# Kernel optimization log

Measured on AMD Instinct MI355X. Metric: run time of the kernel, lower is better.

The kernel has to match this reference:

```python
import jax, jax.numpy as jnp
import numpy as np
import math

B, Q_LEN, K_LEN = 8, 512, 512
D_MODEL, H = 512, 8
DK = D_MODEL // H


def setup_inputs() -> dict:
    key = jax.random.key(0)
    ks = jax.random.split(key, 12)
    inp = {
        "query": jax.random.normal(ks[0], (B, Q_LEN, D_MODEL), jnp.float32),
        "key": jax.random.normal(ks[1], (B, K_LEN, D_MODEL), jnp.float32),
        "value": jax.random.normal(ks[2], (B, K_LEN, D_MODEL), jnp.float32),
        "relative_embeddings": jax.random.normal(ks[3], (K_LEN, Q_LEN, D_MODEL), jnp.float32),
        # causal mask: 1 = attend, 0 = masked
        "mask": jnp.tril(jnp.ones((Q_LEN, K_LEN), dtype=bool)),
        "Wq": jax.random.normal(ks[4], (D_MODEL, D_MODEL), jnp.float32) / math.sqrt(D_MODEL),
        "Wk": jax.random.normal(ks[5], (D_MODEL, D_MODEL), jnp.float32) / math.sqrt(D_MODEL),
        "Wv": jax.random.normal(ks[6], (D_MODEL, D_MODEL), jnp.float32) / math.sqrt(D_MODEL),
        "Wo": jax.random.normal(ks[7], (D_MODEL, D_MODEL), jnp.float32) / math.sqrt(D_MODEL),
        "Wr": jax.random.normal(ks[8], (D_MODEL, D_MODEL), jnp.float32) / math.sqrt(D_MODEL),
        "u": jax.random.normal(ks[9], (H, DK), jnp.float32),
        "v": jax.random.normal(ks[10], (H, DK), jnp.float32),
    }
    return inp


def reference(query, key, value, relative_embeddings, mask, Wq, Wk, Wv, Wo, Wr, u, v):
    b, q_len, d_model = query.shape
    k_len = key.shape[1]
    # torch nn.Linear(x) = x @ W.T (bias=False)
    Qh = (query @ Wq.T).reshape(b, q_len, H, DK).transpose(0, 2, 1, 3)   # bhqd
    Kh = (key @ Wk.T).reshape(b, k_len, H, DK).transpose(0, 2, 1, 3)     # bhkd
    Vh = (value @ Wv.T).reshape(b, k_len, H, DK).transpose(0, 2, 1, 3)   # bhkd
    # relative position projection: (k_len, q_len, d_model)
    R = relative_embeddings @ Wr.T
    # view(k,q,H,dk).permute(2,1,0,3) -> (H, q, k, dk)
    Rh = R.reshape(k_len, q_len, H, DK).transpose(2, 1, 0, 3)
    # content score: (Q + u) K^T
    content = jnp.einsum("bhqd,bhkd->bhqk", Qh + u[None, :, None, :], Kh)
    # position score: (Q + v) R^T, R per-head per-query
    position = jnp.einsum("bhqd,hqkd->bhqk", Qh + v[None, :, None, :], Rh)
    scores = (content + position) / math.sqrt(DK)
    scores = jnp.where(mask[None, None, :, :], scores, -1e9)
    weights = jax.nn.softmax(scores, axis=-1)  # dropout is identity in eval
    out = jnp.einsum("bhqk,bhkd->bhqd", weights, Vh)
    out = out.transpose(0, 2, 1, 3).reshape(b, q_len, d_model)
    out = out @ Wo.T
    return (out, weights)
```

## Files before the change

### kernel.cpp

```cpp
#include <hip/hip_runtime.h>

#define BATCH   8
#define SEQ     512
#define DMODEL  512
#define NHEAD   8
#define DKH     64

typedef __attribute__((ext_vector_type(8))) short bf16x8;
typedef __attribute__((ext_vector_type(4))) float f32x4;

__device__ __forceinline__ short f2bf(float f) {
    union { float f; unsigned u; } v; v.f = f;
    unsigned r = v.u + 0x7FFFu + ((v.u >> 16) & 1u);
    return (short)(r >> 16);
}
__device__ __forceinline__ float bf2f(short s) {
    union { unsigned u; float f; } v; v.u = ((unsigned)(unsigned short)s) << 16;
    return v.f;
}

#define LDK 40

__device__ __forceinline__ void stage_f32(const float* __restrict__ base,
                                          int rstride, short* lds, int tid) {
    int r = tid >> 2, c = (tid & 3) << 3;
    const float* p = base + (size_t)r * rstride + c;
    float4 x = *(const float4*)p;
    float4 y = *(const float4*)(p + 4);
    union { short s[8]; bf16x8 v; } o;
    o.s[0] = f2bf(x.x); o.s[1] = f2bf(x.y); o.s[2] = f2bf(x.z); o.s[3] = f2bf(x.w);
    o.s[4] = f2bf(y.x); o.s[5] = f2bf(y.y); o.s[6] = f2bf(y.z); o.s[7] = f2bf(y.w);
    *(bf16x8*)(lds + r * LDK + c) = o.v;
}

__device__ __forceinline__ void stage_bf16(const short* __restrict__ base,
                                           int rstride, short* lds, int tid) {
    int r = tid >> 2, c = (tid & 3) << 3;
    bf16x8 v = *(const bf16x8*)(base + (size_t)r * rstride + c);
    *(bf16x8*)(lds + r * LDK + c) = v;
}

__device__ __forceinline__ void mma_tile(const short* As, const short* Bs,
                                         int lane, int wm, int wn, f32x4 acc[2][2]) {
    int lo = lane & 15, hi = lane >> 4;
    bf16x8 a0 = *(const bf16x8*)(As + (wm * 32 + lo) * LDK + hi * 8);
    bf16x8 a1 = *(const bf16x8*)(As + (wm * 32 + 16 + lo) * LDK + hi * 8);
    bf16x8 b0 = *(const bf16x8*)(Bs + (wn * 32 + lo) * LDK + hi * 8);
    bf16x8 b1 = *(const bf16x8*)(Bs + (wn * 32 + 16 + lo) * LDK + hi * 8);
    acc[0][0] = __builtin_amdgcn_mfma_f32_16x16x32_bf16(a0, b0, acc[0][0], 0, 0, 0);
    acc[0][1] = __builtin_amdgcn_mfma_f32_16x16x32_bf16(a0, b1, acc[0][1], 0, 0, 0);
    acc[1][0] = __builtin_amdgcn_mfma_f32_16x16x32_bf16(a1, b0, acc[1][0], 0, 0, 0);
    acc[1][1] = __builtin_amdgcn_mfma_f32_16x16x32_bf16(a1, b1, acc[1][1], 0, 0, 0);
}

__global__ __launch_bounds__(256) void qkvw_kernel(
        const float* __restrict__ query, const float* __restrict__ key_,
        const float* __restrict__ value,
        const float* __restrict__ Wq, const float* __restrict__ Wk,
        const float* __restrict__ Wv, const float* __restrict__ Wr,
        const float* __restrict__ uvec, const float* __restrict__ vvec,
        short* __restrict__ Qu, short* __restrict__ Qv,
        short* __restrict__ Kh, short* __restrict__ Vt,
        short* __restrict__ Wrt) {
    __shared__ short As[64 * LDK], Bs[64 * LDK];
    int f = blockIdx.x, tid = threadIdx.x;
    if (f >= 1536) {
        int base = (f - 1536) * 1024;
        #pragma unroll
        for (int j = 0; j < 4; j++) {
            int idx = base + j * 256 + tid;
            int n = idx >> 9, m = idx & 511;
            Wrt[idx] = f2bf(Wr[(size_t)m * 512 + n]);
        }
        return;
    }
    int i = f >> 3;
    int nt = i & 7;
    int gm = (f & 7) * 24 + (i >> 3);
    int mode = gm >> 6, mt = gm & 63;
    const float* x = mode == 0 ? query : (mode == 1 ? key_ : value);
    const float* W = mode == 0 ? Wq : (mode == 1 ? Wk : Wv);
    int lane = tid & 63, w = tid >> 6, wm = w >> 1, wn = w & 1;
    const float* Abase = x + (size_t)mt * 64 * DMODEL;
    const float* Bbase = W + (size_t)nt * 64 * DMODEL;
    f32x4 acc[2][2] = {};
    for (int kt = 0; kt < DMODEL; kt += 32) {
        __syncthreads();
        stage_f32(Abase + kt, DMODEL, As, tid);
        stage_f32(Bbase + kt, DMODEL, Bs, tid);
        __syncthreads();
        mma_tile(As, Bs, lane, wm, wn, acc);
    }
    int lo = lane & 15, hi = lane >> 4;
    for (int fm = 0; fm < 2; fm++)
        for (int fn = 0; fn < 2; fn++)
            for (int r = 0; r < 4; r++) {
                int m = mt * 64 + wm * 32 + fm * 16 + hi * 4 + r;
                int n = nt * 64 + wn * 32 + fn * 16 + lo;
                float val = acc[fm][fn][r];
                int b = m >> 9, s = m & 511, h = n >> 6, d = n & 63;
                if (mode == 0) {
                    size_t idx = ((size_t)(b * NHEAD + h) * SEQ + s) * DKH + d;
                    Qu[idx] = f2bf(val + uvec[n]);
                    Qv[idx] = f2bf(val + vvec[n]);
                } else if (mode == 1) {
                    Kh[((size_t)(b * NHEAD + h) * SEQ + s) * DKH + d] = f2bf(val);
                } else {
                    Vt[((size_t)(b * NHEAD + h) * DKH + d) * SEQ + s] = f2bf(val);
                }
            }
}

__global__ __launch_bounds__(256) void tc_kernel(const short* __restrict__ Qv,
                                                 const short* __restrict__ Wrt,
                                                 short* __restrict__ T2,
                                                 const short* __restrict__ Qu,
                                                 const short* __restrict__ Kh,
                                                 float* __restrict__ scores) {
    __shared__ short As[64 * LDK], Bs[64 * LDK];
    int f0 = blockIdx.x, tid = threadIdx.x;
    int lane = tid & 63, w = tid >> 6, wm = w >> 1, wn = w & 1;
    int lo = lane & 15, hi = lane >> 4;
    if (f0 < 4096) {
        int f = f0;
        int i = f >> 3;
        int nt = i & 7;
        int mh = (f & 7) * 64 + (i >> 3);
        int mt = mh >> 3, h = mh & 7;
        int m0 = mt * 64, b = m0 >> 9, q0 = m0 & 511;
        const short* Abase = Qv + ((size_t)(b * NHEAD + h) * SEQ + q0) * DKH;
        const short* Bbase = Wrt + (size_t)nt * 64 * DMODEL + h * DKH;
        f32x4 acc[2][2] = {};
        for (int kt = 0; kt < DKH; kt += 32) {
            __syncthreads();
            stage_bf16(Abase + kt, DKH, As, tid);
            stage_bf16(Bbase + kt, DMODEL, Bs, tid);
            __syncthreads();
            mma_tile(As, Bs, lane, wm, wn, acc);
        }
        int bh = b * NHEAD + h;
        for (int fm = 0; fm < 2; fm++)
            for (int fn = 0; fn < 2; fn++)
                for (int r = 0; r < 4; r++) {
                    int q = q0 + wm * 32 + fm * 16 + hi * 4 + r;
                    int n = nt * 64 + wn * 32 + fn * 16 + lo;
                    T2[((size_t)q * 64 + bh) * DMODEL + n] = f2bf(acc[fm][fn][r]);
                }
    } else {
        int i = f0 - 4096;
        int x = i & 7, j = i >> 3;
        int bhl = j / 36, t = j % 36;
        int bh = x * 8 + bhl;
        int qt = 0, base = 0;
        #pragma unroll
        for (int s = 1; s <= 7; s++) { if (t >= base + qt + 1) { base += qt + 1; qt++; } }
        int kt_ = t - base;
        const short* Abase = Qu + ((size_t)bh * SEQ + qt * 64) * DKH;
        const short* Bbase = Kh + ((size_t)bh * SEQ + kt_ * 64) * DKH;
        f32x4 acc[2][2] = {};
        for (int kt = 0; kt < DKH; kt += 32) {
            __syncthreads();
            stage_bf16(Abase + kt, DKH, As, tid);
            stage_bf16(Bbase + kt, DKH, Bs, tid);
            __syncthreads();
            mma_tile(As, Bs, lane, wm, wn, acc);
        }
        for (int fm = 0; fm < 2; fm++)
            for (int fn = 0; fn < 2; fn++)
                for (int r = 0; r < 4; r++) {
                    int q = qt * 64 + wm * 32 + fm * 16 + hi * 4 + r;
                    int k = kt_ * 64 + wn * 32 + fn * 16 + lo;
                    scores[((size_t)bh * SEQ + q) * SEQ + k] = acc[fm][fn][r];
                }
    }
}

__global__ __launch_bounds__(1024) void position_kernel(const short* __restrict__ T2,
                                                        const float* __restrict__ rel,
                                                        float* __restrict__ scores) {
    int bk = blockIdx.x;
    int x = bk & 7, idx = bk >> 3;
    int q = (idx < 32) ? (idx * 8 + x) : (511 - ((idx - 32) * 8 + x));
    __shared__ short Tl[64 * 512];
    int tid = threadIdx.x, w = tid >> 6, lane = tid & 63;
    const short* Tq = T2 + (size_t)q * (64 * DMODEL);
    #pragma unroll
    for (int it = 0; it < 4; ++it) {
        int chunk = it * 1024 + tid;
        int r = chunk >> 6, c = chunk & 63;
        bf16x8 v = *(const bf16x8*)(Tq + (size_t)chunk * 8);
        *(bf16x8*)(Tl + r * 512 + (c ^ (r & 7)) * 8) = v;
    }
    __syncthreads();
    int kbase = w * 32;
    if (kbase > q) return;
    int lo = lane & 15, hi = lane >> 4;
    const float* relq = rel + ((size_t)kbase * SEQ + q) * DMODEL;
    f32x4 acc[4][2] = {};
    for (int n = 0; n < DMODEL; n += 32) {
        bf16x8 a[4];
        #pragma unroll
        for (int fm = 0; fm < 4; fm++) {
            int rr = fm * 16 + lo;
            int g = ((n >> 3) + hi) ^ (rr & 7);
            a[fm] = *(const bf16x8*)(Tl + rr * 512 + g * 8);
        }
        bf16x8 bfrag[2];
        #pragma unroll
        for (int fk = 0; fk < 2; fk++) {
            const float* p = relq + (size_t)(fk * 16 + lo) * (SEQ * DMODEL) + n + hi * 8;
            float4 xv = *(const float4*)p;
            float4 yv = *(const float4*)(p + 4);
            union { short s[8]; bf16x8 v; } o;
            o.s[0] = f2bf(xv.x); o.s[1] = f2bf(xv.y); o.s[2] = f2bf(xv.z); o.s[3] = f2bf(xv.w);
            o.s[4] = f2bf(yv.x); o.s[5] = f2bf(yv.y); o.s[6] = f2bf(yv.z); o.s[7] = f2bf(yv.w);
            bfrag[fk] = o.v;
        }
        #pragma unroll
        for (int fm = 0; fm < 4; fm++) {
            acc[fm][0] = __builtin_amdgcn_mfma_f32_16x16x32_bf16(a[fm], bfrag[0], acc[fm][0], 0, 0, 0);
            acc[fm][1] = __builtin_amdgcn_mfma_f32_16x16x32_bf16(a[fm], bfrag[1], acc[fm][1], 0, 0, 0);
        }
    }
    #pragma unroll
    for (int fm = 0; fm < 4; fm++)
        #pragma unroll
        for (int fk = 0; fk < 2; fk++)
            #pragma unroll
            for (int r = 0; r < 4; r++) {
                int bh = fm * 16 + hi * 4 + r;
                int k = kbase + fk * 16 + lo;
                scores[((size_t)bh * SEQ + q) * SEQ + k] += acc[fm][fk][r];
            }
}

#define PSTR 520
__global__ __launch_bounds__(256) void pv_sm_kernel(float* __restrict__ scores,
                                                    const short* __restrict__ Vt,
                                                    short* __restrict__ attn) {
    __shared__ short Ps[64 * PSTR];
    __shared__ float invS_lds[64];
    int f = blockIdx.x;
    int i = f >> 3;
    int bhl, qt;
    if (i < 32) { bhl = i >> 3;            qt = i & 7; }
    else        { bhl = 4 + ((i - 32) >> 3); qt = 7 - (i & 7); }
    int bh = (f & 7) * 8 + bhl;
    int tid = threadIdx.x, lane = tid & 63, w = tid >> 6, wm = w >> 1, wn = w & 1;
    int kmax = (qt + 1) * 64;
    int r = tid >> 2, c4 = tid & 3;
    int q = qt * 64 + r;
    int cc = c4 * 8;
    float* row = scores + ((size_t)bh * SEQ + q) * SEQ;
    float S = 0.f;
    for (int kt = 0; kt < kmax; kt += 32) {
        float4 x = *(const float4*)(row + kt + cc);
        float4 y = *(const float4*)(row + kt + cc + 4);
        float p0 = (kt + cc + 0 <= q) ? __expf(x.x * 0.125f) : 0.f;
        float p1 = (kt + cc + 1 <= q) ? __expf(x.y * 0.125f) : 0.f;
        float p2 = (kt + cc + 2 <= q) ? __expf(x.z * 0.125f) : 0.f;
        float p3 = (kt + cc + 3 <= q) ? __expf(x.w * 0.125f) : 0.f;
        float p4 = (kt + cc + 4 <= q) ? __expf(y.x * 0.125f) : 0.f;
        float p5 = (kt + cc + 5 <= q) ? __expf(y.y * 0.125f) : 0.f;
        float p6 = (kt + cc + 6 <= q) ? __expf(y.z * 0.125f) : 0.f;
        float p7 = (kt + cc + 7 <= q) ? __expf(y.w * 0.125f) : 0.f;
        S += p0 + p1 + p2 + p3 + p4 + p5 + p6 + p7;
        union { short s[8]; bf16x8 v; } o;
        o.s[0] = f2bf(p0); o.s[1] = f2bf(p1); o.s[2] = f2bf(p2); o.s[3] = f2bf(p3);
        o.s[4] = f2bf(p4); o.s[5] = f2bf(p5); o.s[6] = f2bf(p6); o.s[7] = f2bf(p7);
        *(bf16x8*)(Ps + r * PSTR + kt + cc) = o.v;
    }
    S += __shfl_xor(S, 1); S += __shfl_xor(S, 2);
    float invS = 1.0f / S;
    if (c4 == 0) invS_lds[r] = invS;
    for (int kt = 0; kt < SEQ; kt += 32) {
        float4 o0, o1;
        if (kt < kmax) {
            const short* pr = Ps + r * PSTR + kt + cc;
            o0 = make_float4(bf2f(pr[0]) * invS, bf2f(pr[1]) * invS,
                             bf2f(pr[2]) * invS, bf2f(pr[3]) * invS);
            o1 = make_float4(bf2f(pr[4]) * invS, bf2f(pr[5]) * invS,
                             bf2f(pr[6]) * invS, bf2f(pr[7]) * invS);
        } else {
            o0 = make_float4(0.f, 0.f, 0.f, 0.f); o1 = o0;
        }
        *(float4*)(row + kt + cc) = o0;
        *(float4*)(row + kt + cc + 4) = o1;
    }
    __syncthreads();
    const short* Vtb = Vt + (size_t)bh * DKH * SEQ;
    int lo = lane & 15, hi = lane >> 4;
    f32x4 acc[2][2] = {};
    for (int kc = 0; kc < kmax; kc += 32) {
        bf16x8 a0 = *(const bf16x8*)(Ps + (wm * 32 + lo) * PSTR + kc + hi * 8);
        bf16x8 a1 = *(const bf16x8*)(Ps + (wm * 32 + 16 + lo) * PSTR + kc + hi * 8);
        bf16x8 b0 = *(const bf16x8*)(Vtb + (size_t)(wn * 32 + lo) * SEQ + kc + hi * 8);
        bf16x8 b1 = *(const bf16x8*)(Vtb + (size_t)(wn * 32 + 16 + lo) * SEQ + kc + hi * 8);
        acc[0][0] = __builtin_amdgcn_mfma_f32_16x16x32_bf16(a0, b0, acc[0][0], 0, 0, 0);
        acc[0][1] = __builtin_amdgcn_mfma_f32_16x16x32_bf16(a0, b1, acc[0][1], 0, 0, 0);
        acc[1][0] = __builtin_amdgcn_mfma_f32_16x16x32_bf16(a1, b0, acc[1][0], 0, 0, 0);
        acc[1][1] = __builtin_amdgcn_mfma_f32_16x16x32_bf16(a1, b1, acc[1][1], 0, 0, 0);
    }
    int b = bh >> 3, h = bh & 7;
    for (int fm = 0; fm < 2; fm++)
        for (int fn = 0; fn < 2; fn++)
            for (int rr = 0; rr < 4; rr++) {
                int ql = wm * 32 + fm * 16 + hi * 4 + rr;
                int d = wn * 32 + fn * 16 + lo;
                float val = acc[fm][fn][rr] * invS_lds[ql];
                attn[((size_t)b * SEQ + qt * 64 + ql) * DMODEL + h * DKH + d] = f2bf(val);
            }
}

__global__ __launch_bounds__(256) void oproj_kernel(const short* __restrict__ attn,
                                                    const float* __restrict__ Wo,
                                                    float* __restrict__ out) {
    __shared__ short As[64 * LDK], Bs[64 * LDK];
    int f = blockIdx.x;
    int i = f >> 3;
    int mt = (f & 7) * 8 + (i >> 3);
    int nt = i & 7;
    int tid = threadIdx.x, lane = tid & 63, w = tid >> 6, wm = w >> 1, wn = w & 1;
    const short* Abase = attn + (size_t)mt * 64 * DMODEL;
    const float* Bbase = Wo + (size_t)nt * 64 * DMODEL;
    f32x4 acc[2][2] = {};
    for (int kt = 0; kt < DMODEL; kt += 32) {
        __syncthreads();
        stage_bf16(Abase + kt, DMODEL, As, tid);
        stage_f32(Bbase + kt, DMODEL, Bs, tid);
        __syncthreads();
        mma_tile(As, Bs, lane, wm, wn, acc);
    }
    int lo = lane & 15, hi = lane >> 4;
    for (int fm = 0; fm < 2; fm++)
        for (int fn = 0; fn < 2; fn++)
            for (int r = 0; r < 4; r++) {
                int m = mt * 64 + wm * 32 + fm * 16 + hi * 4 + r;
                int n = nt * 64 + wn * 32 + fn * 16 + lo;
                out[(size_t)m * DMODEL + n] = acc[fm][fn][r];
            }
}

extern "C" void kernel_launch(void* const* d_in, const int* in_sizes, int n_in,
                              void* d_out, int out_size, void* d_ws, size_t ws_size,
                              hipStream_t stream) {
    (void)in_sizes; (void)n_in; (void)out_size; (void)ws_size;
    const float* query = (const float*)d_in[0];
    const float* key   = (const float*)d_in[1];
    const float* value = (const float*)d_in[2];
    const float* rel   = (const float*)d_in[3];
    const float* Wq = (const float*)d_in[5];
    const float* Wk = (const float*)d_in[6];
    const float* Wv = (const float*)d_in[7];
    const float* Wo = (const float*)d_in[8];
    const float* Wr = (const float*)d_in[9];
    const float* u  = (const float*)d_in[10];
    const float* v  = (const float*)d_in[11];

    float* out     = (float*)d_out;
    float* weights = out + (size_t)BATCH * SEQ * DMODEL;

    char* ws = (char*)d_ws;
    short* Qu   = (short*)(ws);
    short* Qv   = (short*)(ws + ((size_t)4 << 20));
    short* Kh   = (short*)(ws + ((size_t)8 << 20));
    short* Vt   = (short*)(ws + ((size_t)12 << 20));
    short* T2   = (short*)(ws + ((size_t)16 << 20));
    short* attn = (short*)(ws + ((size_t)48 << 20));
    short* Wrt  = (short*)(ws + ((size_t)52 << 20));

    qkvw_kernel<<<1792, 256, 0, stream>>>(query, key, value, Wq, Wk, Wv, Wr,
                                          u, v, Qu, Qv, Kh, Vt, Wrt);
    tc_kernel<<<6400, 256, 0, stream>>>(Qv, Wrt, T2, Qu, Kh, weights);
    position_kernel<<<512, 1024, 0, stream>>>(T2, rel, weights);
    pv_sm_kernel<<<512, 256, 0, stream>>>(weights, Vt, attn);
    oproj_kernel<<<512, 256, 0, stream>>>(attn, Wo, out);
}
```

Before: 192.4 us.

## Loop over N tiles inside tc_kernel blocks, reusing the staged A tile in registers

Each tc_kernel block now loads its 64x64 Q tile once, keeps its MFMA fragments in registers, and loops over all output column tiles (8 Wr tiles, or the causal K tiles up to qt), instead of launching one block per output tile. The grid shrinks from 6400 to 1024 blocks, which removes repeated A-tile loads and per-block launch overhead. The causal branch pairs short and long q-tile rows so the uneven work balances across blocks. The cost is less parallelism, since each block runs a longer serial loop with two barriers per iteration and no overlap between loads and compute.

```diff
diff --git a/kernel.cpp b/kernel.cpp
--- a/kernel.cpp
+++ b/kernel.cpp
@@ -117,61 +117,91 @@
                                                  const short* __restrict__ Qu,
                                                  const short* __restrict__ Kh,
                                                  float* __restrict__ scores) {
-    __shared__ short As[64 * LDK], Bs[64 * LDK];
+    __shared__ short As[2 * 64 * LDK], Bs[2 * 64 * LDK];
     int f0 = blockIdx.x, tid = threadIdx.x;
     int lane = tid & 63, w = tid >> 6, wm = w >> 1, wn = w & 1;
     int lo = lane & 15, hi = lane >> 4;
-    if (f0 < 4096) {
-        int f = f0;
-        int i = f >> 3;
-        int nt = i & 7;
-        int mh = (f & 7) * 64 + (i >> 3);
+    if (f0 < 512) {
+        int x = f0 & 7, i = f0 >> 3;
+        int mh = x * 64 + i;
         int mt = mh >> 3, h = mh & 7;
         int m0 = mt * 64, b = m0 >> 9, q0 = m0 & 511;
+        int bh = b * NHEAD + h;
         const short* Abase = Qv + ((size_t)(b * NHEAD + h) * SEQ + q0) * DKH;
-        const short* Bbase = Wrt + (size_t)nt * 64 * DMODEL + h * DKH;
-        f32x4 acc[2][2] = {};
-        for (int kt = 0; kt < DKH; kt += 32) {
+        stage_bf16(Abase + 0,  DKH, As,            tid);
+        stage_bf16(Abase + 32, DKH, As + 64 * LDK, tid);
+        __syncthreads();
+        bf16x8 aq[2][2];
+        #pragma unroll
+        for (int ch = 0; ch < 2; ch++) {
+            aq[ch][0] = *(const bf16x8*)(As + ch * 64 * LDK + (wm * 32 + lo) * LDK + hi * 8);
+            aq[ch][1] = *(const bf16x8*)(As + ch * 64 * LDK + (wm * 32 + 16 + lo) * LDK + hi * 8);
+        }
+        for (int nt = 0; nt < 8; nt++) {
+            const short* Bbase = Wrt + (size_t)nt * 64 * DMODEL + h * DKH;
             __syncthreads();
-            stage_bf16(Abase + kt, DKH, As, tid);
-            stage_bf16(Bbase + kt, DMODEL, Bs, tid);
+            stage_bf16(Bbase + 0,  DMODEL, Bs,            tid);
+            stage_bf16(Bbase + 32, DMODEL, Bs + 64 * LDK, tid);
             __syncthreads();
-            mma_tile(As, Bs, lane, wm, wn, acc);
-        }
-        int bh = b * NHEAD + h;
-        for (int fm = 0; fm < 2; fm++)
-            for (int fn = 0; fn < 2; fn++)
-                for (int r = 0; r < 4; r++) {
-                    int q = q0 + wm * 32 + fm * 16 + hi * 4 + r;
-                    int n = nt * 64 + wn * 32 + fn * 16 + lo;
-                    T2[((size_t)q * 64 + bh) * DMODEL + n] = f2bf(acc[fm][fn][r]);
-                }
+            f32x4 acc[2][2] = {};
+            #pragma unroll
+            for (int ch = 0; ch < 2; ch++) {
+                bf16x8 b0 = *(const bf16x8*)(Bs + ch * 64 * LDK + (wn * 32 + lo) * LDK + hi * 8);
+                bf16x8 b1 = *(const bf16x8*)(Bs + ch * 64 * LDK + (wn * 32 + 16 + lo) * LDK + hi * 8);
+                acc[0][0] = __builtin_amdgcn_mfma_f32_16x16x32_bf16(aq[ch][0], b0, acc[0][0], 0, 0, 0);
+                acc[0][1] = __builtin_amdgcn_mfma_f32_16x16x32_bf16(aq[ch][0], b1, acc[0][1], 0, 0, 0);
+                acc[1][0] = __builtin_amdgcn_mfma_f32_16x16x32_bf16(aq[ch][1], b0, acc[1][0], 0, 0, 0);
+                acc[1][1] = __builtin_amdgcn_mfma_f32_16x16x32_bf16(aq[ch][1], b1, acc[1][1], 0, 0, 0);
+            }
+            for (int fm = 0; fm < 2; fm++)
+                for (int fn = 0; fn < 2; fn++)
+                    for (int r = 0; r < 4; r++) {
+                        int q = q0 + wm * 32 + fm * 16 + hi * 4 + r;
+                        int n = nt * 64 + wn * 32 + fn * 16 + lo;
+                        T2[((size_t)q * 64 + bh) * DMODEL + n] = f2bf(acc[fm][fn][r]);
+                    }
+        }
     } else {
-        int i = f0 - 4096;
-        int x = i & 7, j = i >> 3;
-        int bhl = j / 36, t = j % 36;
+        int fi = f0 - 512;
+        int x = fi & 7, i = fi >> 3;
+        int bhl, qt;
+        if (i < 32) { bhl = i >> 3;              qt = i & 7; }
+        else        { bhl = 4 + ((i - 32) >> 3); qt = 7 - (i & 7); }
         int bh = x * 8 + bhl;
-        int qt = 0, base = 0;
-        #pragma unroll
-        for (int s = 1; s <= 7; s++) { if (t >= base + qt + 1) { base += qt + 1; qt++; } }
-        int kt_ = t - base;
         const short* Abase = Qu + ((size_t)bh * SEQ + qt * 64) * DKH;
-        const short* Bbase = Kh + ((size_t)bh * SEQ + kt_ * 64) * DKH;
-        f32x4 acc[2][2] = {};
-        for (int kt = 0; kt < DKH; kt += 32) {
+        stage_bf16(Abase + 0,  DKH, As,            tid);
+        stage_bf16(Abase + 32, DKH, As + 64 * LDK, tid);
+        __syncthreads();
+        bf16x8 aq[2][2];
+        #pragma unroll
+        for (int ch = 0; ch < 2; ch++) {
+            aq[ch][0] = *(const bf16x8*)(As + ch * 64 * LDK + (wm * 32 + lo) * LDK + hi * 8);
+            aq[ch][1] = *(const bf16x8*)(As + ch * 64 * LDK + (wm * 32 + 16 + lo) * LDK + hi * 8);
+        }
+        for (int kt_ = 0; kt_ <= qt; kt_++) {
+            const short* Bbase = Kh + ((size_t)bh * SEQ + kt_ * 64) * DKH;
             __syncthreads();
-            stage_bf16(Abase + kt, DKH, As, tid);
-            stage_bf16(Bbase + kt, DKH, Bs, tid);
+            stage_bf16(Bbase + 0,  DKH, Bs,            tid);
+            stage_bf16(Bbase + 32, DKH, Bs + 64 * LDK, tid);
             __syncthreads();
-            mma_tile(As, Bs, lane, wm, wn, acc);
-        }
-        for (int fm = 0; fm < 2; fm++)
-            for (int fn = 0; fn < 2; fn++)
-                for (int r = 0; r < 4; r++) {
-                    int q = qt * 64 + wm * 32 + fm * 16 + hi * 4 + r;
-                    int k = kt_ * 64 + wn * 32 + fn * 16 + lo;
-                    scores[((size_t)bh * SEQ + q) * SEQ + k] = acc[fm][fn][r];
-                }
+            f32x4 acc[2][2] = {};
+            #pragma unroll
+            for (int ch = 0; ch < 2; ch++) {
+                bf16x8 b0 = *(const bf16x8*)(Bs + ch * 64 * LDK + (wn * 32 + lo) * LDK + hi * 8);
+                bf16x8 b1 = *(const bf16x8*)(Bs + ch * 64 * LDK + (wn * 32 + 16 + lo) * LDK + hi * 8);
+                acc[0][0] = __builtin_amdgcn_mfma_f32_16x16x32_bf16(aq[ch][0], b0, acc[0][0], 0, 0, 0);
+                acc[0][1] = __builtin_amdgcn_mfma_f32_16x16x32_bf16(aq[ch][0], b1, acc[0][1], 0, 0, 0);
+                acc[1][0] = __builtin_amdgcn_mfma_f32_16x16x32_bf16(aq[ch][1], b0, acc[1][0], 0, 0, 0);
+                acc[1][1] = __builtin_amdgcn_mfma_f32_16x16x32_bf16(aq[ch][1], b1, acc[1][1], 0, 0, 0);
+            }
+            for (int fm = 0; fm < 2; fm++)
+                for (int fn = 0; fn < 2; fn++)
+                    for (int r = 0; r < 4; r++) {
+                        int q = qt * 64 + wm * 32 + fm * 16 + hi * 4 + r;
+                        int k = kt_ * 64 + wn * 32 + fn * 16 + lo;
+                        scores[((size_t)bh * SEQ + q) * SEQ + k] = acc[fm][fn][r];
+                    }
+        }
     }
 }
 
@@ -371,7 +401,7 @@
 
     qkvw_kernel<<<1792, 256, 0, stream>>>(query, key, value, Wq, Wk, Wv, Wr,
                                           u, v, Qu, Qv, Kh, Vt, Wrt);
-    tc_kernel<<<6400, 256, 0, stream>>>(Qv, Wrt, T2, Qu, Kh, weights);
+    tc_kernel<<<1024, 256, 0, stream>>>(Qv, Wrt, T2, Qu, Kh, weights);
     position_kernel<<<512, 1024, 0, stream>>>(T2, rel, weights);
     pv_sm_kernel<<<512, 256, 0, stream>>>(weights, Vt, attn);
     oproj_kernel<<<512, 256, 0, stream>>>(attn, Wo, out);
```

Result: no change. 193.1 us (+0.4%).
